# Performance work log

Measured on AMD Instinct MI355X. Metric: run time of the kernel, lower is better.

The kernel has to match this reference:

```python
import jax, jax.numpy as jnp
import numpy as np

DPW = 1.0       # dist_push_weight
IW = 1.0        # intensity_weight
MINDIST = 0.05
MAXVAL = 255.0
KS = 11         # gaussian blur kernel size


def _gaussian_blur(img):
    """torchvision-style gaussian_blur with kernel_size=11, default sigma, reflect pad. img: [B,H,W]."""
    sigma = 0.3 * ((KS - 1) * 0.5 - 1) + 0.8  # = 2.0
    half = (KS - 1) * 0.5
    x = jnp.linspace(-half, half, KS)
    pdf = jnp.exp(-0.5 * (x / sigma) ** 2)
    k1 = (pdf / pdf.sum()).astype(img.dtype)
    pad = KS // 2
    xp = jnp.pad(img, ((0, 0), (pad, pad), (pad, pad)), mode='reflect')
    lhs = xp[:, None]  # [B,1,H+2p,W+2p]
    kh = k1.reshape(1, 1, KS, 1)
    kw = k1.reshape(1, 1, 1, KS)
    y = jax.lax.conv_general_dilated(lhs, kh, (1, 1), 'VALID')
    y = jax.lax.conv_general_dilated(y, kw, (1, 1), 'VALID')
    return y[:, 0]


def _dist_push(tr):
    """tr: [N,2]. mean over upper-triangle pairs of clamp(mindist - dist, 0)."""
    n = tr.shape[0]
    sq = jnp.sum(tr * tr, axis=-1)                       # [N]
    d2 = sq[:, None] + sq[None, :] - 2.0 * (tr @ tr.T)   # [N,N]
    d2 = jnp.maximum(d2, 0.0)
    mask = jnp.triu(jnp.ones((n, n), dtype=bool), k=1)
    d = jnp.sqrt(jnp.where(mask, d2, 1.0))               # safe sqrt off-mask
    vals = jnp.where(mask, jnp.maximum(MINDIST - d, 0.0), 0.0)
    npairs = n * (n - 1) // 2
    return jnp.sum(vals) / npairs


def _intensity(x, trace):
    """x: [H,W] blurred image, trace: [N,2] in [0,1]. Returns per-point bilinear-ish intensity [N]."""
    H, W = x.shape
    idx0 = trace[:, 0] * H
    idx1 = trace[:, 1] * W
    xp = jnp.pad(x, ((0, 2), (0, 2)), mode='reflect')    # reflect pad right/bottom by 2
    i0 = jax.lax.stop_gradient(jnp.floor(idx0 + 0.5))
    i1 = i0 + 1.0
    j0 = jax.lax.stop_gradient(jnp.floor(idx1 + 0.5))
    j1 = j0 + 1.0
    i0i = i0.astype(jnp.int32); i1i = i1.astype(jnp.int32)
    j0i = j0.astype(jnp.int32); j1i = j1.astype(jnp.int32)
    y00 = xp[i0i, j0i]
    y10 = xp[i1i, j0i]
    y01 = xp[i0i, j1i]
    out_ax0 = (i1 - idx0) * y00 + (idx0 - i0) * y10
    out_ax1 = (j1 - idx1) * y00 + (idx1 - j0) * y01
    return (out_ax0 + out_ax1) / 2.0


def setup_inputs() -> dict:
    key = jax.random.key(0)
    k1, k2 = jax.random.split(key)
    trace = jax.random.uniform(k1, (8, 4096, 2), dtype=jnp.float32)
    img = jax.random.uniform(k2, (8, 512, 512), dtype=jnp.float32)
    return {"trace": trace, "img": img}


def reference(trace, img):
    dist_push_loss = jnp.mean(jax.vmap(_dist_push)(trace))
    imgf = _gaussian_blur(img)
    intensity = jax.vmap(_intensity)(imgf, trace)   # [B,N]
    int_loss = jnp.mean(MAXVAL - intensity)
    return dist_push_loss * DPW + int_loss * IW
```

## Files before the change

### kernel.cpp

```cpp
#include <hip/hip_runtime.h>

#define IMW 512
#define NP 4096

#define NROW 20
#define DIST_BLOCKS 160
#define GATHER_BLOCKS 256
#define TOTAL_BLOCKS (DIST_BLOCKS + GATHER_BLOCKS)
#define BS 256

__device__ constexpr float KW[11] = {
    0.00881223f, 0.02714359f, 0.06511407f, 0.12164908f, 0.17699836f,
    0.20056542f, 0.17699836f, 0.12164908f, 0.06511407f, 0.02714359f, 0.00881223f};

__device__ __forceinline__ int refl(int r) {
    r = r < 0 ? -r : r;
    return r > 511 ? 1022 - r : r;
}

__global__ __launch_bounds__(BS)
void fused_compute(const float* __restrict__ trace, const float* __restrict__ img,
                   float* __restrict__ partials) {
    const int tid = threadIdx.x;
    const int bx = blockIdx.x;
    const int lane = tid & 63;

    __shared__ __align__(16) char smem[49184];
    float2* band = (float2*)smem;
    int* cidx = (int*)(smem + 32768);
    int* cnts = (int*)(smem + 49152);
    float* red = (float*)(smem + 49160);

    float local;

    if (bx < DIST_BLOCKS) {
        const int b = bx / NROW, row = bx - b * NROW;
        const float2* tb = (const float2*)(trace + b * NP * 2);
        if (tid == 0) { cnts[0] = 0; cnts[1] = 0; }
        __syncthreads();
        for (int k = tid; k < NP; k += BS) {
            const float2 pt = tb[k];
            const int cy = min((int)(pt.y * 20.f), NROW - 1);
            const bool inb = (cy >= row - 1) && (cy <= row + 1);
            const bool isc = (cy == row);
            const unsigned long long mb = __ballot(inb);
            const unsigned long long pre = mb & ((1ull << lane) - 1ull);
            int base = 0;
            if (lane == 0) base = atomicAdd(&cnts[0], __popcll(mb));
            base = __shfl(base, 0, 64);
            const int pos = base + __popcll(pre);
            if (inb) band[pos] = pt;
            const unsigned long long mc = __ballot(isc);
            int cbase = 0;
            if (lane == 0) cbase = atomicAdd(&cnts[1], __popcll(mc));
            cbase = __shfl(cbase, 0, 64);
            if (isc) cidx[cbase + __popcll(mc & ((1ull << lane) - 1ull))] = pos;
        }
        __syncthreads();
        const int nb = cnts[0], nc = cnts[1];
        float s = 0.f;
        for (int c = tid; c < nc; c += BS) {
            const float2 p = band[cidx[c]];
            float acc = 0.f;
            for (int q = 0; q < nb; ++q) {
                const float2 o = band[q];
                const float dx = p.x - o.x, dy = p.y - o.y;
                const float d2 = fmaf(dx, dx, dy * dy);
                acc += (d2 < 0.0025f) ? (0.05f - __builtin_amdgcn_sqrtf(d2)) : 0.f;
            }
            s += acc;
        }
        local = s;
    } else {
        const int g = bx - DIST_BLOCKS;
        const int half = tid & 1;
        const int p = g * 128 + (tid >> 1);
        const int b = p >> 12;
        const float2 t2 = ((const float2*)trace)[b * NP + (p & (NP - 1))];
        const float idx0 = t2.x * 512.f, idx1 = t2.y * 512.f;
        const float i0f = floorf(idx0 + 0.5f), j0f = floorf(idx1 + 0.5f);
        const float wi = idx0 - i0f, wj = idx1 - j0f;
        const int i0 = (int)i0f, j0 = (int)j0f;
        const int mi0 = refl(i0), mi1 = refl(i0 + 1);
        const int mj0 = refl(j0), mj1 = refl(j0 + 1);
        const int ilo = min(mi0, mi1), jlo = min(mj0, mj1);
        const bool sr = mi0 > mi1, sc = mj0 > mj1;
        const float* srcb = img + b * (IMW * IMW);

        int cc[12];
#pragma unroll
        for (int c = 0; c < 12; ++c) cc[c] = refl(jlo - 5 + c);

        float A_lo = 0.f, A_hi = 0.f, B_lo = 0.f, B_hi = 0.f;
#pragma unroll
        for (int rr = 0; rr < 6; ++rr) {
            const int r = half ? rr + 6 : rr;
            const float* base = srcb + refl(ilo - 5 + r) * IMW;
            float lo = 0.f, hi = 0.f;
#pragma unroll
            for (int c = 0; c < 12; ++c) {
                const float v = base[cc[c]];
                if (c < 11) lo = fmaf(KW[c], v, lo);
                if (c > 0) hi = fmaf(KW[c - 1], v, hi);
            }
            const float wlo = half ? (rr < 5 ? KW[rr + 6] : 0.f) : KW[rr];
            const float whi = half ? KW[rr + 5] : (rr > 0 ? KW[rr - 1] : 0.f);
            A_lo = fmaf(wlo, lo, A_lo);
            A_hi = fmaf(whi, lo, A_hi);
            B_lo = fmaf(wlo, hi, B_lo);
            B_hi = fmaf(whi, hi, B_hi);
        }
        A_lo += __shfl_xor(A_lo, 1, 64);
        A_hi += __shfl_xor(A_hi, 1, 64);
        B_lo += __shfl_xor(B_lo, 1, 64);
        B_hi += __shfl_xor(B_hi, 1, 64);
        const float yA  = sr ? A_hi : A_lo;
        const float yA1 = sr ? A_lo : A_hi;
        const float yB  = sr ? B_hi : B_lo;
        const float yB1 = sr ? B_lo : B_hi;
        const float y00 = sc ? yB : yA;
        const float y01 = sc ? yA : yB;
        const float y10 = sc ? yB1 : yA1;
        const float inten = 0.5f * ((1.f - wi) * y00 + wi * y10 + (1.f - wj) * y00 + wj * y01);
        local = (half == 0) ? inten : 0.f;
    }

    for (int o = 32; o; o >>= 1) local += __shfl_down(local, o, 64);
    __syncthreads();
    if ((tid & 63) == 0) red[tid >> 6] = local;
    __syncthreads();
    if (tid == 0) partials[bx] = red[0] + red[1] + red[2] + red[3];
}

__global__ __launch_bounds__(256)
void finalize(const float* __restrict__ partials, float* __restrict__ out) {
    const int tid = threadIdx.x;
    float sg = 0.f, sd = 0.f;
    for (int i = tid; i < TOTAL_BLOCKS; i += 256) {
        const float v = partials[i];
        if (i < DIST_BLOCKS) sd += v; else sg += v;
    }
    for (int o = 32; o; o >>= 1) {
        sg += __shfl_down(sg, o, 64);
        sd += __shfl_down(sd, o, 64);
    }
    __shared__ float rg[4], rd[4];
    if ((tid & 63) == 0) { rg[tid >> 6] = sg; rd[tid >> 6] = sd; }
    __syncthreads();
    if (tid == 0) {
        const double Sd = (double)(rd[0] + rd[1] + rd[2] + rd[3]);
        const double S1 = (double)(rg[0] + rg[1] + rg[2] + rg[3]);
        const double dp = (Sd - 1638.4) / 134184960.0;
        const double il = 255.0 - S1 / 32768.0;
        out[0] = (float)(dp + il);
    }
}

extern "C" void kernel_launch(void* const* d_in, const int* in_sizes, int n_in,
                              void* d_out, int out_size, void* d_ws, size_t ws_size,
                              hipStream_t stream) {
    const float* trace = (const float*)d_in[0];
    const float* img = (const float*)d_in[1];
    float* partials = (float*)d_ws;
    float* out = (float*)d_out;

    fused_compute<<<TOTAL_BLOCKS, BS, 0, stream>>>(trace, img, partials);
    finalize<<<1, 256, 0, stream>>>(partials, out);
}
```

Measured before the change: 94.76 us.

## Precompute full vertical blur into workspace, then gather with horizontal-only pass

```diff
diff --git a/kernel.cpp b/kernel.cpp
--- a/kernel.cpp
+++ b/kernel.cpp
@@ -5,8 +5,9 @@
 
 #define NROW 20
 #define DIST_BLOCKS 160
-#define GATHER_BLOCKS 256
-#define TOTAL_BLOCKS (DIST_BLOCKS + GATHER_BLOCKS)
+#define VB_BLOCKS 2048
+#define K1_BLOCKS (DIST_BLOCKS + VB_BLOCKS)
+#define GATHER_BLOCKS 128
 #define BS 256
 
 __device__ constexpr float KW[11] = {
@@ -19,112 +20,70 @@
 }
 
 __global__ __launch_bounds__(BS)
-void fused_compute(const float* __restrict__ trace, const float* __restrict__ img,
-                   float* __restrict__ partials) {
+void k1_dist_vblur(const float* __restrict__ trace, const float* __restrict__ img,
+                   float* __restrict__ ws1, float* __restrict__ partials) {
     const int tid = threadIdx.x;
     const int bx = blockIdx.x;
+
+    if (bx >= DIST_BLOCKS) {
+        const int idx = (bx - DIST_BLOCKS) * BS + tid;
+        const int w4 = idx & 127, h = (idx >> 7) & 511, b = idx >> 16;
+        const float4* ib4 = (const float4*)(img + b * (IMW * IMW));
+        float4 a = make_float4(0.f, 0.f, 0.f, 0.f);
+#pragma unroll
+        for (int t = 0; t < 11; ++t) {
+            const float4 v = ib4[refl(h - 5 + t) * 128 + w4];
+            a.x = fmaf(KW[t], v.x, a.x);
+            a.y = fmaf(KW[t], v.y, a.y);
+            a.z = fmaf(KW[t], v.z, a.z);
+            a.w = fmaf(KW[t], v.w, a.w);
+        }
+        ((float4*)ws1)[idx] = a;
+        return;
+    }
+
     const int lane = tid & 63;
-
     __shared__ __align__(16) char smem[49184];
     float2* band = (float2*)smem;
     int* cidx = (int*)(smem + 32768);
     int* cnts = (int*)(smem + 49152);
     float* red = (float*)(smem + 49160);
 
-    float local;
-
-    if (bx < DIST_BLOCKS) {
-        const int b = bx / NROW, row = bx - b * NROW;
-        const float2* tb = (const float2*)(trace + b * NP * 2);
-        if (tid == 0) { cnts[0] = 0; cnts[1] = 0; }
-        __syncthreads();
-        for (int k = tid; k < NP; k += BS) {
-            const float2 pt = tb[k];
-            const int cy = min((int)(pt.y * 20.f), NROW - 1);
-            const bool inb = (cy >= row - 1) && (cy <= row + 1);
-            const bool isc = (cy == row);
-            const unsigned long long mb = __ballot(inb);
-            const unsigned long long pre = mb & ((1ull << lane) - 1ull);
-            int base = 0;
-            if (lane == 0) base = atomicAdd(&cnts[0], __popcll(mb));
-            base = __shfl(base, 0, 64);
-            const int pos = base + __popcll(pre);
-            if (inb) band[pos] = pt;
-            const unsigned long long mc = __ballot(isc);
-            int cbase = 0;
-            if (lane == 0) cbase = atomicAdd(&cnts[1], __popcll(mc));
-            cbase = __shfl(cbase, 0, 64);
-            if (isc) cidx[cbase + __popcll(mc & ((1ull << lane) - 1ull))] = pos;
+    const int b = bx / NROW, row = bx - b * NROW;
+    const float2* tb = (const float2*)(trace + b * NP * 2);
+    if (tid == 0) { cnts[0] = 0; cnts[1] = 0; }
+    __syncthreads();
+    for (int k = tid; k < NP; k += BS) {
+        const float2 pt = tb[k];
+        const int cy = min((int)(pt.y * 20.f), NROW - 1);
+        const bool inb = (cy >= row - 1) && (cy <= row + 1);
+        const bool isc = (cy == row);
+        const unsigned long long mb = __ballot(inb);
+        int base = 0;
+        if (lane == 0) base = atomicAdd(&cnts[0], __popcll(mb));
+        base = __shfl(base, 0, 64);
+        const int pos = base + __popcll(mb & ((1ull << lane) - 1ull));
+        if (inb) band[pos] = pt;
+        const unsigned long long mc = __ballot(isc);
+        int cbase = 0;
+        if (lane == 0) cbase = atomicAdd(&cnts[1], __popcll(mc));
+        cbase = __shfl(cbase, 0, 64);
+        if (isc) cidx[cbase + __popcll(mc & ((1ull << lane) - 1ull))] = pos;
+    }
+    __syncthreads();
+    const int nb = cnts[0], nc = cnts[1];
+    float local = 0.f;
+    for (int c = tid; c < nc; c += BS) {
+        const float2 p = band[cidx[c]];
+        float acc = 0.f;
+        for (int q = 0; q < nb; ++q) {
+            const float2 o = band[q];
+            const float dx = p.x - o.x, dy = p.y - o.y;
+            const float d2 = fmaf(dx, dx, dy * dy);
+            acc += (d2 < 0.0025f) ? (0.05f - __builtin_amdgcn_sqrtf(d2)) : 0.f;
         }
-        __syncthreads();
-        const int nb = cnts[0], nc = cnts[1];
-        float s = 0.f;
-        for (int c = tid; c < nc; c += BS) {
-            const float2 p = band[cidx[c]];
-            float acc = 0.f;
-            for (int q = 0; q < nb; ++q) {
-                const float2 o = band[q];
-                const float dx = p.x - o.x, dy = p.y - o.y;
-                const float d2 = fmaf(dx, dx, dy * dy);
-                acc += (d2 < 0.0025f) ? (0.05f - __builtin_amdgcn_sqrtf(d2)) : 0.f;
-            }
-            s += acc;
-        }
-        local = s;
-    } else {
-        const int g = bx - DIST_BLOCKS;
-        const int half = tid & 1;
-        const int p = g * 128 + (tid >> 1);
-        const int b = p >> 12;
-        const float2 t2 = ((const float2*)trace)[b * NP + (p & (NP - 1))];
-        const float idx0 = t2.x * 512.f, idx1 = t2.y * 512.f;
-        const float i0f = floorf(idx0 + 0.5f), j0f = floorf(idx1 + 0.5f);
-        const float wi = idx0 - i0f, wj = idx1 - j0f;
-        const int i0 = (int)i0f, j0 = (int)j0f;
-        const int mi0 = refl(i0), mi1 = refl(i0 + 1);
-        const int mj0 = refl(j0), mj1 = refl(j0 + 1);
-        const int ilo = min(mi0, mi1), jlo = min(mj0, mj1);
-        const bool sr = mi0 > mi1, sc = mj0 > mj1;
-        const float* srcb = img + b * (IMW * IMW);
-
-        int cc[12];
-#pragma unroll
-        for (int c = 0; c < 12; ++c) cc[c] = refl(jlo - 5 + c);
-
-        float A_lo = 0.f, A_hi = 0.f, B_lo = 0.f, B_hi = 0.f;
-#pragma unroll
-        for (int rr = 0; rr < 6; ++rr) {
-            const int r = half ? rr + 6 : rr;
-            const float* base = srcb + refl(ilo - 5 + r) * IMW;
-            float lo = 0.f, hi = 0.f;
-#pragma unroll
-            for (int c = 0; c < 12; ++c) {
-                const float v = base[cc[c]];
-                if (c < 11) lo = fmaf(KW[c], v, lo);
-                if (c > 0) hi = fmaf(KW[c - 1], v, hi);
-            }
-            const float wlo = half ? (rr < 5 ? KW[rr + 6] : 0.f) : KW[rr];
-            const float whi = half ? KW[rr + 5] : (rr > 0 ? KW[rr - 1] : 0.f);
-            A_lo = fmaf(wlo, lo, A_lo);
-            A_hi = fmaf(whi, lo, A_hi);
-            B_lo = fmaf(wlo, hi, B_lo);
-            B_hi = fmaf(whi, hi, B_hi);
-        }
-        A_lo += __shfl_xor(A_lo, 1, 64);
-        A_hi += __shfl_xor(A_hi, 1, 64);
-        B_lo += __shfl_xor(B_lo, 1, 64);
-        B_hi += __shfl_xor(B_hi, 1, 64);
-        const float yA  = sr ? A_hi : A_lo;
-        const float yA1 = sr ? A_lo : A_hi;
-        const float yB  = sr ? B_hi : B_lo;
-        const float yB1 = sr ? B_lo : B_hi;
-        const float y00 = sc ? yB : yA;
-        const float y01 = sc ? yA : yB;
-        const float y10 = sc ? yB1 : yA1;
-        const float inten = 0.5f * ((1.f - wi) * y00 + wi * y10 + (1.f - wj) * y00 + wj * y01);
-        local = (half == 0) ? inten : 0.f;
+        local += acc;
     }
-
     for (int o = 32; o; o >>= 1) local += __shfl_down(local, o, 64);
     __syncthreads();
     if ((tid & 63) == 0) red[tid >> 6] = local;
@@ -132,11 +91,58 @@
     if (tid == 0) partials[bx] = red[0] + red[1] + red[2] + red[3];
 }
 
-__global__ __launch_bounds__(256)
+__global__ __launch_bounds__(BS)
+void k2_gather(const float* __restrict__ trace, const float* __restrict__ vb,
+               float* __restrict__ partials) {
+    const int tid = threadIdx.x;
+    const int bx = blockIdx.x;
+    const int p = bx * BS + tid;
+    const int b = p >> 12;
+    const float2 t2 = ((const float2*)trace)[b * NP + (p & (NP - 1))];
+    const float idx0 = t2.x * 512.f, idx1 = t2.y * 512.f;
+    const float i0f = floorf(idx0 + 0.5f), j0f = floorf(idx1 + 0.5f);
+    const float wi = idx0 - i0f, wj = idx1 - j0f;
+    const int i0 = (int)i0f, j0 = (int)j0f;
+    const int mi0 = refl(i0), mi1 = refl(i0 + 1);
+    const int mj0 = refl(j0), mj1 = refl(j0 + 1);
+    const int jlo = min(mj0, mj1);
+    const bool sc = mj0 > mj1;
+    const float* srcb = vb + b * (IMW * IMW);
+    const float* r0 = srcb + mi0 * IMW;
+    const float* r1 = srcb + mi1 * IMW;
+
+    float v0[12], v1[12];
+#pragma unroll
+    for (int c = 0; c < 12; ++c) {
+        const int cc = refl(jlo - 5 + c);
+        v0[c] = r0[cc];
+        v1[c] = r1[cc];
+    }
+    float y00lo = 0.f, y00hi = 0.f, y10lo = 0.f, y10hi = 0.f;
+#pragma unroll
+    for (int c = 0; c < 11; ++c) {
+        y00lo = fmaf(KW[c], v0[c], y00lo);
+        y00hi = fmaf(KW[c], v0[c + 1], y00hi);
+        y10lo = fmaf(KW[c], v1[c], y10lo);
+        y10hi = fmaf(KW[c], v1[c + 1], y10hi);
+    }
+    const float y00 = sc ? y00hi : y00lo;
+    const float y01 = sc ? y00lo : y00hi;
+    const float y10 = sc ? y10hi : y10lo;
+    float local = 0.5f * ((1.f - wi) * y00 + wi * y10 + (1.f - wj) * y00 + wj * y01);
+
+    __shared__ float red[4];
+    for (int o = 32; o; o >>= 1) local += __shfl_down(local, o, 64);
+    if ((tid & 63) == 0) red[tid >> 6] = local;
+    __syncthreads();
+    if (tid == 0) partials[DIST_BLOCKS + bx] = red[0] + red[1] + red[2] + red[3];
+}
+
+__global__ __launch_bounds__(BS)
 void finalize(const float* __restrict__ partials, float* __restrict__ out) {
     const int tid = threadIdx.x;
     float sg = 0.f, sd = 0.f;
-    for (int i = tid; i < TOTAL_BLOCKS; i += 256) {
+    for (int i = tid; i < DIST_BLOCKS + GATHER_BLOCKS; i += BS) {
         const float v = partials[i];
         if (i < DIST_BLOCKS) sd += v; else sg += v;
     }
@@ -162,8 +168,10 @@
     const float* trace = (const float*)d_in[0];
     const float* img = (const float*)d_in[1];
     float* partials = (float*)d_ws;
+    float* ws1 = (float*)((char*)d_ws + 4096);
     float* out = (float*)d_out;
 
-    fused_compute<<<TOTAL_BLOCKS, BS, 0, stream>>>(trace, img, partials);
-    finalize<<<1, 256, 0, stream>>>(partials, out);
+    k1_dist_vblur<<<K1_BLOCKS, BS, 0, stream>>>(trace, img, ws1, partials);
+    k2_gather<<<GATHER_BLOCKS, BS, 0, stream>>>(trace, ws1, partials);
+    finalize<<<1, BS, 0, stream>>>(partials, out);
 }
```

Measured after the change: 100.4 us. 1.06x slower.
